# Optimization experiments

Hardware: AMD Instinct MI355X
Metric: run time of the kernel (lower is better)

Reference implementation:

```python
import jax, jax.numpy as jnp
import numpy as np

B, T, D = 256, 512, 32   # batch, seq_len, var_length (== input_size == output_size)
H, L = 256, 2            # hidden_size, num_layers


def setup_inputs() -> dict:
    key = jax.random.key(0)
    ks = jax.random.split(key, 16)
    s = 1.0 / np.sqrt(H)  # PyTorch LSTM/Linear default init range
    def u(k, shape):
        return jax.random.uniform(k, shape, jnp.float32, -s, s)
    inp = {"input": jax.random.normal(ks[0], (B, T, D), jnp.float32)}
    # encoder LSTM (b = b_ih + b_hh folded together); gate order i,f,g,o
    inp["enc_Wih0"] = u(ks[1], (4 * H, D)); inp["enc_Whh0"] = u(ks[2], (4 * H, H)); inp["enc_b0"] = u(ks[3], (4 * H,))
    inp["enc_Wih1"] = u(ks[4], (4 * H, H)); inp["enc_Whh1"] = u(ks[5], (4 * H, H)); inp["enc_b1"] = u(ks[6], (4 * H,))
    # decoder LSTM
    inp["dec_Wih0"] = u(ks[7], (4 * H, D)); inp["dec_Whh0"] = u(ks[8], (4 * H, H)); inp["dec_b0"] = u(ks[9], (4 * H,))
    inp["dec_Wih1"] = u(ks[10], (4 * H, H)); inp["dec_Whh1"] = u(ks[11], (4 * H, H)); inp["dec_b1"] = u(ks[12], (4 * H,))
    # output projection
    inp["fc_W"] = u(ks[13], (D, H)); inp["fc_b"] = u(ks[14], (D,))
    return inp


def _lstm_cell(x, h, c, Wih, Whh, b):
    g = x @ Wih.T + h @ Whh.T + b            # [B, 4H]
    i, f, gg, o = jnp.split(g, 4, axis=-1)   # PyTorch gate order i,f,g,o
    c = jax.nn.sigmoid(f) * c + jax.nn.sigmoid(i) * jnp.tanh(gg)
    h = jax.nn.sigmoid(o) * jnp.tanh(c)
    return h, c


def reference(input, enc_Wih0, enc_Whh0, enc_b0, enc_Wih1, enc_Whh1, enc_b1,
              dec_Wih0, dec_Whh0, dec_b0, dec_Wih1, dec_Whh1, dec_b1, fc_W, fc_b):
    b, t, d = input.shape
    hdim = enc_Whh0.shape[1]
    x = jnp.transpose(input, (1, 0, 2))  # time-major [T, B, D]

    # ----- encoder: 2-layer LSTM, keep final (h, c) per layer -----
    enc = [(enc_Wih0, enc_Whh0, enc_b0), (enc_Wih1, enc_Whh1, enc_b1)]
    hs, cs = [], []
    seq = x
    for Wih, Whh, bb in enc:
        def step(carry, xt, Wih=Wih, Whh=Whh, bb=bb):
            h, c = carry
            h, c = _lstm_cell(xt, h, c, Wih, Whh, bb)
            return (h, c), h
        z = jnp.zeros((b, hdim), input.dtype)
        (hT, cT), seq = jax.lax.scan(step, (z, z), seq)
        hs.append(hT); cs.append(cT)
    h0 = jnp.stack(hs)  # [L, B, H]
    c0 = jnp.stack(cs)

    dec = [(dec_Wih0, dec_Whh0, dec_b0), (dec_Wih1, dec_Whh1, dec_b1)]

    def dec_step(carry, _):
        xt, h, c = carry
        inp_l = xt
        new_h, new_c = [], []
        for l, (Wih, Whh, bb) in enumerate(dec):
            hl, cl = _lstm_cell(inp_l, h[l], c[l], Wih, Whh, bb)
            new_h.append(hl); new_c.append(cl)
            inp_l = hl
        pred = inp_l @ fc_W.T + fc_b  # [B, D]
        return (pred, jnp.stack(new_h), jnp.stack(new_c)), pred

    x0 = jnp.zeros((b, d), input.dtype)
    _, preds = jax.lax.scan(dec_step, (x0, h0, c0), None, length=t)  # [T, B, D]
    # cat along time then reverse (inv_idx)
    out = jnp.transpose(preds, (1, 0, 2))[:, ::-1, :]
    return out
```

## Files before the change

kernel.cpp:

```cpp
#include <hip/hip_runtime.h>

typedef __attribute__((ext_vector_type(8))) short bf16x8;
typedef __attribute__((ext_vector_type(4))) float f32x4;

#define MFMA16(a,b,c) __builtin_amdgcn_mfma_f32_16x16x32_bf16((a),(b),(c),0,0,0)


#define SZ_HBUF   (2*256*256*2)
#define OFF_H0H   0
#define OFF_H0L   (OFF_H0H + SZ_HBUF)
#define OFF_H1H   (OFF_H0L + SZ_HBUF)
#define OFF_H1L   (OFF_H1H + SZ_HBUF)
#define OFF_CFIN  (OFF_H1L + SZ_HBUF)
#define OFF_EW0H  (OFF_CFIN + 524288)
#define OFF_EW0L  (OFF_EW0H + 589824)
#define OFF_EW1H  (OFF_EW0L + 589824)
#define OFF_EW1L  (OFF_EW1H + 1048576)
#define OFF_DW0H  (OFF_EW1L + 1048576)
#define OFF_DW0L  (OFF_DW0H + 1048576)
#define OFF_DW1H  (OFF_DW0L + 1048576)
#define OFF_DW1L  (OFF_DW1H + 1048576)
#define OFF_BEFF  (OFF_DW1L + 1048576)
#define OFF_FCWH  (OFF_BEFF + 4096)
#define OFF_FCWL  (OFF_FCWH + 16384)
#define OFF_EFLG  (OFF_FCWL + 16384)
#define OFF_DFLG  (OFF_EFLG + 4096)

static __device__ __forceinline__ unsigned short f2bf(float f) {
  unsigned u = __float_as_uint(f);
  u = u + 0x7fffu + ((u >> 16) & 1u);
  return (unsigned short)(u >> 16);
}
static __device__ __forceinline__ float bf2f(unsigned short s) {
  return __uint_as_float(((unsigned)s) << 16);
}
static __device__ __forceinline__ float sigf(float x) {
  return 1.f / (1.f + __expf(-x));
}
static __device__ __forceinline__ float tanhsafe(float x) {
  float a = fabsf(x);
  float e = __expf(-2.f * a);
  float t = (1.f - e) / (1.f + e);
  return x < 0.f ? -t : t;
}
static __device__ __forceinline__ void st_hpair(float h, unsigned short* ph, unsigned short* pl) {
  unsigned short hi = f2bf(h);
  unsigned short lo = f2bf(h - bf2f(hi));
  __hip_atomic_store(ph, hi, __ATOMIC_RELAXED, __HIP_MEMORY_SCOPE_AGENT);
  __hip_atomic_store(pl, lo, __ATOMIC_RELAXED, __HIP_MEMORY_SCOPE_AGENT);
}
static __device__ __forceinline__ f32x4 ld16(const void* p) {
  f32x4 d;
  asm volatile("global_load_dwordx4 %0, %1, off sc0 sc1" : "=&v"(d) : "v"(p) : "memory");
  return d;
}
static __device__ __forceinline__ void wait_vm0() {
  asm volatile("s_waitcnt vmcnt(0)" ::: "memory");
  __builtin_amdgcn_sched_barrier(0);
}
static __device__ __forceinline__ void flag_barrier(unsigned* flags, int gc, unsigned round) {
  __syncthreads();
  if (threadIdx.x == 0)
    __hip_atomic_store(flags + gc, round, __ATOMIC_RELAXED, __HIP_MEMORY_SCOPE_AGENT);
  if (threadIdx.x < 64) {
    int l = threadIdx.x;
    for (;;) {
      unsigned v = (l < 16) ? __hip_atomic_load(flags + l, __ATOMIC_RELAXED, __HIP_MEMORY_SCOPE_AGENT)
                            : round;
      if (__all((int)(v >= round))) break;
    }
  }
  __syncthreads();
}

#define LDSF(base, row, kk) \
  (*(const bf16x8*)((base) + ((((row) << 9) | (lrow << 4) | ((kk) << 6)) ^ (((row) & 7) << 4))))

__global__ void k_prep_cat(int nrows, const float* __restrict__ s0, int K0,
                           const float* __restrict__ s1, int K1,
                           unsigned short* __restrict__ whi, unsigned short* __restrict__ wlo) {
  int K = K0 + K1;
  int tot = nrows * K;
  for (int idx = blockIdx.x * blockDim.x + threadIdx.x; idx < tot; idx += gridDim.x * blockDim.x) {
    int n = idx / K, k = idx - n * K;
    float v = (k < K0) ? s0[n * K0 + k] : s1[n * K1 + (k - K0)];
    unsigned short hi = f2bf(v);
    unsigned short lo = f2bf(v - bf2f(hi));
    whi[idx] = hi; wlo[idx] = lo;
  }
}
__global__ void k_prep_dec0(const float* __restrict__ Wih0, const float* __restrict__ Whh0,
                            const float* __restrict__ fcW,
                            unsigned short* __restrict__ whi, unsigned short* __restrict__ wlo) {
  int tot = 1024 * 512;
  for (int idx = blockIdx.x * blockDim.x + threadIdx.x; idx < tot; idx += gridDim.x * blockDim.x) {
    int n = idx >> 9, k = idx & 511;
    float v;
    if (k < 256) {
      v = 0.f;
      #pragma unroll
      for (int d = 0; d < 32; ++d) v += Wih0[n * 32 + d] * fcW[d * 256 + k];
    } else {
      v = Whh0[n * 256 + (k - 256)];
    }
    unsigned short hi = f2bf(v);
    unsigned short lo = f2bf(v - bf2f(hi));
    whi[idx] = hi; wlo[idx] = lo;
  }
}
__global__ void k_prep_beff(const float* __restrict__ Wih0, const float* __restrict__ b0,
                            const float* __restrict__ fcb, float* __restrict__ beff) {
  int n = blockIdx.x * blockDim.x + threadIdx.x;
  if (n < 1024) {
    float v = b0[n];
    #pragma unroll
    for (int d = 0; d < 32; ++d) v += Wih0[n * 32 + d] * fcb[d];
    beff[n] = v;
  }
}

__global__ __launch_bounds__(256, 1)
void k_encoder(const float* __restrict__ input,
               const unsigned short* __restrict__ w0hi, const unsigned short* __restrict__ w0lo,
               const unsigned short* __restrict__ w1hi, const unsigned short* __restrict__ w1lo,
               const float* __restrict__ b0, const float* __restrict__ b1,
               unsigned short* h0h, unsigned short* h0l,
               unsigned short* h1h, unsigned short* h1l,
               float* __restrict__ cfin, unsigned* flags)
{
  const int wg = blockIdx.x;
  const int gb = wg & 15, gc = wg >> 4;
  const int tid = threadIdx.x;
  const int wid = tid >> 6, lane = tid & 63;
  const int lcol = lane & 15, lrow = lane >> 4;
  const int r0 = gb * 16, u0 = gc * 16;
  const int wrow = wid * 256 + u0 + lcol;

  __shared__ char s_h0[2][8192];
  __shared__ char s_h1[2][8192];
  __shared__ float gA[4][16][17];
  __shared__ float gB[4][16][17];
  __shared__ float cb[2][16][16];

  cb[0][tid >> 4][tid & 15] = 0.f;
  cb[1][tid >> 4][tid & 15] = 0.f;

  const int srow = (tid >> 5) & 7;
  const int scol8 = (tid & 31) << 3;
  const int dA = ((srow << 9) | ((tid & 31) << 4)) ^ (srow << 4);
  const int dB = dA + 4096;

  bf16x8 w0h_[9], w0l_[9], w1h_[16], w1l_[16];
  {
    const unsigned short* p = w0hi + (size_t)wrow * 288 + lrow * 8;
    const unsigned short* q = w0lo + (size_t)wrow * 288 + lrow * 8;
    #pragma unroll
    for (int kk = 0; kk < 9; ++kk) {
      w0h_[kk] = *(const bf16x8*)(p + kk * 32);
      w0l_[kk] = *(const bf16x8*)(q + kk * 32);
    }
    const unsigned short* p1 = w1hi + (size_t)wrow * 512 + lrow * 8;
    const unsigned short* q1 = w1lo + (size_t)wrow * 512 + lrow * 8;
    #pragma unroll
    for (int kk = 0; kk < 16; ++kk) {
      w1h_[kk] = *(const bf16x8*)(p1 + kk * 32);
      w1l_[kk] = *(const bf16x8*)(q1 + kk * 32);
    }
  }
  const float bias0 = b0[wrow];
  const float bias1 = b1[wrow];
  unsigned* gflags = flags + gb * 64;
  __syncthreads();

  for (int k = 0; k <= 512; ++k) {
    const int rp = (k - 1) & 1;
    const int wp = k & 1;

    f32x4 ahh = {0.f,0.f,0.f,0.f}, ahl = {0.f,0.f,0.f,0.f}, alh = {0.f,0.f,0.f,0.f};
    union { bf16x8 v; unsigned short s[8]; } xh, xl;
    if (k < 512) {
      const float* px = input + (size_t)(r0 + lcol) * 16384 + (size_t)k * 32 + lrow * 8;
      f32x4 a = *(const f32x4*)px;
      f32x4 b = *(const f32x4*)(px + 4);
      #pragma unroll
      for (int j = 0; j < 4; ++j) {
        unsigned short t1 = f2bf(a[j]); xh.s[j] = t1;     xl.s[j]     = f2bf(a[j] - bf2f(t1));
        unsigned short t2 = f2bf(b[j]); xh.s[4 + j] = t2; xl.s[4 + j] = f2bf(b[j] - bf2f(t2));
      }
    }

    const unsigned short* p0h = h0h + (size_t)rp * 65536 + (size_t)(r0 + srow) * 256 + scol8;
    const unsigned short* p0l = h0l + (size_t)rp * 65536 + (size_t)(r0 + srow) * 256 + scol8;
    const unsigned short* p1h = h1h + (size_t)wp * 65536 + (size_t)(r0 + srow) * 256 + scol8;
    const unsigned short* p1l = h1l + (size_t)wp * 65536 + (size_t)(r0 + srow) * 256 + scol8;
    f32x4 v0 = ld16(p0h), v1 = ld16(p0h + 2048);
    f32x4 v2 = ld16(p0l), v3 = ld16(p0l + 2048);
    f32x4 v4 = ld16(p1h), v5 = ld16(p1h + 2048);
    f32x4 v6 = ld16(p1l), v7 = ld16(p1l + 2048);

    if (k < 512) {
      ahh = MFMA16(xh.v, w0h_[0], ahh);
      ahl = MFMA16(xh.v, w0l_[0], ahl);
      alh = MFMA16(xl.v, w0h_[0], alh);
    }

    wait_vm0();
    *(f32x4*)(s_h0[0] + dA) = v0; *(f32x4*)(s_h0[0] + dB) = v1;
    *(f32x4*)(s_h0[1] + dA) = v2; *(f32x4*)(s_h0[1] + dB) = v3;
    *(f32x4*)(s_h1[0] + dA) = v4; *(f32x4*)(s_h1[0] + dB) = v5;
    *(f32x4*)(s_h1[1] + dA) = v6; *(f32x4*)(s_h1[1] + dB) = v7;
    __syncthreads();

    bf16x8 f0h[8], f0l[8];
    #pragma unroll
    for (int kk = 0; kk < 8; ++kk) {
      f0h[kk] = LDSF(s_h0[0], lcol, kk);
      f0l[kk] = LDSF(s_h0[1], lcol, kk);
    }

    if (k < 512) {
      #pragma unroll
      for (int kk = 0; kk < 8; ++kk) {
        ahh = MFMA16(f0h[kk], w0h_[kk + 1], ahh);
        ahl = MFMA16(f0h[kk], w0l_[kk + 1], ahl);
        alh = MFMA16(f0l[kk], w0h_[kk + 1], alh);
      }
      f32x4 g = ahh + ahl + alh;
      #pragma unroll
      for (int r = 0; r < 4; ++r) gA[wid][lrow * 4 + r][lcol] = g[r] + bias0;
    }
    if (k >= 1) {
      f32x4 bhh = {0.f,0.f,0.f,0.f}, bhl = {0.f,0.f,0.f,0.f}, blh = {0.f,0.f,0.f,0.f};
      #pragma unroll
      for (int kk = 0; kk < 8; ++kk) {
        bhh = MFMA16(f0h[kk], w1h_[kk], bhh);
        bhl = MFMA16(f0h[kk], w1l_[kk], bhl);
        blh = MFMA16(f0l[kk], w1h_[kk], blh);
      }
      #pragma unroll
      for (int kk = 0; kk < 8; ++kk) {
        bf16x8 fh_ = LDSF(s_h1[0], lcol, kk);
        bf16x8 fl_ = LDSF(s_h1[1], lcol, kk);
        bhh = MFMA16(fh_, w1h_[kk + 8], bhh);
        bhl = MFMA16(fh_, w1l_[kk + 8], bhl);
        blh = MFMA16(fl_, w1h_[kk + 8], blh);
      }
      f32x4 g = bhh + bhl + blh;
      #pragma unroll
      for (int r = 0; r < 4; ++r) gB[wid][lrow * 4 + r][lcol] = g[r] + bias1;
    }
    __syncthreads();

    const int urow = tid >> 4, uu = tid & 15;
    if (k < 512) {
      float gi = gA[0][urow][uu], gf = gA[1][urow][uu];
      float gg = gA[2][urow][uu], go = gA[3][urow][uu];
      float c = sigf(gf) * cb[0][urow][uu] + sigf(gi) * tanhsafe(gg);
      cb[0][urow][uu] = c;
      float h = sigf(go) * tanhsafe(c);
      size_t off = (size_t)wp * 65536 + (size_t)(r0 + urow) * 256 + (u0 + uu);
      st_hpair(h, h0h + off, h0l + off);
    }
    if (k >= 1) {
      float gi = gB[0][urow][uu], gf = gB[1][urow][uu];
      float gg = gB[2][urow][uu], go = gB[3][urow][uu];
      float c = sigf(gf) * cb[1][urow][uu] + sigf(gi) * tanhsafe(gg);
      cb[1][urow][uu] = c;
      float h = sigf(go) * tanhsafe(c);
      size_t off = (size_t)rp * 65536 + (size_t)(r0 + urow) * 256 + (u0 + uu);
      st_hpair(h, h1h + off, h1l + off);
    }
    flag_barrier(gflags, gc, (unsigned)(k + 1));
  }

  const int urow = tid >> 4, uu = tid & 15;
  cfin[(size_t)(r0 + urow) * 256 + (u0 + uu)] = cb[0][urow][uu];
  cfin[65536 + (size_t)(r0 + urow) * 256 + (u0 + uu)] = cb[1][urow][uu];
}

__global__ __launch_bounds__(256, 1)
void k_decoder(const unsigned short* __restrict__ w0hi, const unsigned short* __restrict__ w0lo,
               const unsigned short* __restrict__ w1hi, const unsigned short* __restrict__ w1lo,
               const float* __restrict__ beff, const float* __restrict__ db0,
               const float* __restrict__ b1, const float* __restrict__ fcb,
               const unsigned short* __restrict__ fcwh_g, const unsigned short* __restrict__ fcwl_g,
               unsigned short* h0h, unsigned short* h0l,
               unsigned short* h1h, unsigned short* h1l,
               const float* __restrict__ cfin, float* __restrict__ out, unsigned* flags)
{
  const int wg = blockIdx.x;
  const int gb = wg & 15, gc = wg >> 4;
  const int tid = threadIdx.x;
  const int wid = tid >> 6, lane = tid & 63;
  const int lcol = lane & 15, lrow = lane >> 4;
  const int r0 = gb * 16, u0 = gc * 16;
  const int wrow = wid * 256 + u0 + lcol;

  __shared__ char s_h1[2][8192];
  __shared__ char s_h0[2][2][8192];
  __shared__ char s_fcw[2][16384];
  __shared__ float gA[4][16][17];
  __shared__ float cb[2][16][16];

  const int srow = (tid >> 5) & 7;
  const int scol8 = (tid & 31) << 3;
  const int dA = ((srow << 9) | ((tid & 31) << 4)) ^ (srow << 4);
  const int dB = dA + 4096;

  {
    const int urow = tid >> 4, uu = tid & 15;
    cb[0][urow][uu] = cfin[(size_t)(r0 + urow) * 256 + (u0 + uu)];
    cb[1][urow][uu] = cfin[65536 + (size_t)(r0 + urow) * 256 + (u0 + uu)];
  }
  {
    const unsigned short* q1h = h1h + 65536 + (size_t)(r0 + srow) * 256 + scol8;
    const unsigned short* q1l = h1l + 65536 + (size_t)(r0 + srow) * 256 + scol8;
    const unsigned short* q0h = h0h + 65536 + (size_t)(r0 + srow) * 256 + scol8;
    const unsigned short* q0l = h0l + 65536 + (size_t)(r0 + srow) * 256 + scol8;
    f32x4 v0 = ld16(q1h), v1 = ld16(q1h + 2048);
    f32x4 v2 = ld16(q1l), v3 = ld16(q1l + 2048);
    f32x4 v4 = ld16(q0h), v5 = ld16(q0h + 2048);
    f32x4 v6 = ld16(q0l), v7 = ld16(q0l + 2048);
    f32x4 fh0 = ld16(fcwh_g + (size_t)srow * 256 + scol8);
    f32x4 fh1 = ld16(fcwh_g + (size_t)(srow + 8) * 256 + scol8);
    f32x4 fh2 = ld16(fcwh_g + (size_t)(srow + 16) * 256 + scol8);
    f32x4 fh3 = ld16(fcwh_g + (size_t)(srow + 24) * 256 + scol8);
    f32x4 fl0 = ld16(fcwl_g + (size_t)srow * 256 + scol8);
    f32x4 fl1 = ld16(fcwl_g + (size_t)(srow + 8) * 256 + scol8);
    f32x4 fl2 = ld16(fcwl_g + (size_t)(srow + 16) * 256 + scol8);
    f32x4 fl3 = ld16(fcwl_g + (size_t)(srow + 24) * 256 + scol8);
    wait_vm0();
    *(f32x4*)(s_h1[0] + dA) = v0;    *(f32x4*)(s_h1[0] + dB) = v1;
    *(f32x4*)(s_h1[1] + dA) = v2;    *(f32x4*)(s_h1[1] + dB) = v3;
    *(f32x4*)(s_h0[1][0] + dA) = v4; *(f32x4*)(s_h0[1][0] + dB) = v5;
    *(f32x4*)(s_h0[1][1] + dA) = v6; *(f32x4*)(s_h0[1][1] + dB) = v7;
    *(f32x4*)(s_fcw[0] + dA) = fh0;          *(f32x4*)(s_fcw[0] + dA + 4096) = fh1;
    *(f32x4*)(s_fcw[0] + dA + 8192) = fh2;   *(f32x4*)(s_fcw[0] + dA + 12288) = fh3;
    *(f32x4*)(s_fcw[1] + dA) = fl0;          *(f32x4*)(s_fcw[1] + dA + 4096) = fl1;
    *(f32x4*)(s_fcw[1] + dA + 8192) = fl2;   *(f32x4*)(s_fcw[1] + dA + 12288) = fl3;
  }

  bf16x8 w0h_[16], w0l_[16], w1h_[16], w1l_[16];
  {
    const unsigned short* p = w0hi + (size_t)wrow * 512 + lrow * 8;
    const unsigned short* q = w0lo + (size_t)wrow * 512 + lrow * 8;
    #pragma unroll
    for (int kk = 0; kk < 16; ++kk) {
      w0h_[kk] = *(const bf16x8*)(p + kk * 32);
      w0l_[kk] = *(const bf16x8*)(q + kk * 32);
    }
    const unsigned short* p1 = w1hi + (size_t)wrow * 512 + lrow * 8;
    const unsigned short* q1 = w1lo + (size_t)wrow * 512 + lrow * 8;
    #pragma unroll
    for (int kk = 0; kk < 16; ++kk) {
      w1h_[kk] = *(const bf16x8*)(p1 + kk * 32);
      w1l_[kk] = *(const bf16x8*)(q1 + kk * 32);
    }
  }
  const float bias0 = beff[wrow], bias0t0 = db0[wrow], bias1 = b1[wrow];
  const float fcbv = (wid < 2) ? fcb[wid * 16 + lcol] : 0.f;
  unsigned* gflags = flags + gb * 64;
  __syncthreads();

  bf16x8 h1h_r[8], h1l_r[8];

  for (int t = 0; t < 512; ++t) {
    const int wp = t & 1, rp = 1 - wp;

    f32x4 a0, a1, a2, a3;
    if (t > 0) {
      const unsigned short* ph = h1h + (size_t)rp * 65536 + (size_t)(r0 + srow) * 256 + scol8;
      const unsigned short* pl = h1l + (size_t)rp * 65536 + (size_t)(r0 + srow) * 256 + scol8;
      a0 = ld16(ph); a1 = ld16(ph + 2048);
      a2 = ld16(pl); a3 = ld16(pl + 2048);
    }
    f32x4 ahh = {0.f,0.f,0.f,0.f}, ahl = {0.f,0.f,0.f,0.f}, alh = {0.f,0.f,0.f,0.f};
    #pragma unroll
    for (int kk = 0; kk < 8; ++kk) {
      bf16x8 fh_ = LDSF(s_h0[rp][0], lcol, kk);
      bf16x8 fl_ = LDSF(s_h0[rp][1], lcol, kk);
      ahh = MFMA16(fh_, w0h_[kk + 8], ahh);
      ahl = MFMA16(fh_, w0l_[kk + 8], ahl);
      alh = MFMA16(fl_, w0h_[kk + 8], alh);
    }
    if (t > 0) {
      wait_vm0();
      *(f32x4*)(s_h1[0] + dA) = a0; *(f32x4*)(s_h1[0] + dB) = a1;
      *(f32x4*)(s_h1[1] + dA) = a2; *(f32x4*)(s_h1[1] + dB) = a3;
    }
    __syncthreads();
    #pragma unroll
    for (int kk = 0; kk < 8; ++kk) {
      h1h_r[kk] = LDSF(s_h1[0], lcol, kk);
      h1l_r[kk] = LDSF(s_h1[1], lcol, kk);
    }
    if (t > 0) {
      #pragma unroll
      for (int kk = 0; kk < 8; ++kk) {
        ahh = MFMA16(h1h_r[kk], w0h_[kk], ahh);
        ahl = MFMA16(h1h_r[kk], w0l_[kk], ahl);
        alh = MFMA16(h1l_r[kk], w0h_[kk], alh);
      }
    }
    {
      f32x4 g = ahh + ahl + alh;
      float bb = (t == 0) ? bias0t0 : bias0;
      #pragma unroll
      for (int r = 0; r < 4; ++r) gA[wid][lrow * 4 + r][lcol] = g[r] + bb;
    }
    __syncthreads();
    {
      const int urow = tid >> 4, uu = tid & 15;
      float gi = gA[0][urow][uu], gf = gA[1][urow][uu];
      float gg = gA[2][urow][uu], go = gA[3][urow][uu];
      float c = sigf(gf) * cb[0][urow][uu] + sigf(gi) * tanhsafe(gg);
      cb[0][urow][uu] = c;
      float h = sigf(go) * tanhsafe(c);
      size_t off = (size_t)wp * 65536 + (size_t)(r0 + urow) * 256 + (u0 + uu);
      st_hpair(h, h0h + off, h0l + off);
    }
    flag_barrier(gflags, gc, (unsigned)(2 * t + 1));

    f32x4 b0v, b1v, b2v, b3v;
    {
      const unsigned short* ph = h0h + (size_t)wp * 65536 + (size_t)(r0 + srow) * 256 + scol8;
      const unsigned short* pl = h0l + (size_t)wp * 65536 + (size_t)(r0 + srow) * 256 + scol8;
      b0v = ld16(ph); b1v = ld16(ph + 2048);
      b2v = ld16(pl); b3v = ld16(pl + 2048);
    }
    f32x4 bhh = {0.f,0.f,0.f,0.f}, bhl = {0.f,0.f,0.f,0.f}, blh = {0.f,0.f,0.f,0.f};
    #pragma unroll
    for (int kk = 0; kk < 8; ++kk) {
      bhh = MFMA16(h1h_r[kk], w1h_[kk + 8], bhh);
      bhl = MFMA16(h1h_r[kk], w1l_[kk + 8], bhl);
      blh = MFMA16(h1l_r[kk], w1h_[kk + 8], blh);
    }
    f32x4 p0 = {0.f,0.f,0.f,0.f}, p1 = {0.f,0.f,0.f,0.f}, p2 = {0.f,0.f,0.f,0.f};
    if (t > 0 && wid < 2) {
      #pragma unroll
      for (int kk = 0; kk < 8; ++kk) {
        bf16x8 fh_ = LDSF(s_fcw[0], wid * 16 + lcol, kk);
        bf16x8 fl_ = LDSF(s_fcw[1], wid * 16 + lcol, kk);
        p0 = MFMA16(h1h_r[kk], fh_, p0);
        p1 = MFMA16(h1h_r[kk], fl_, p1);
        p2 = MFMA16(h1l_r[kk], fh_, p2);
      }
    }
    wait_vm0();
    if (t > 0 && wid < 2 && gc == 0) {
      #pragma unroll
      for (int j = 0; j < 4; ++j)
        out[(size_t)(r0 + lrow * 4 + j) * 16384 + (size_t)(512 - t) * 32 + wid * 16 + lcol] =
            p0[j] + p1[j] + p2[j] + fcbv;
    }
    *(f32x4*)(s_h0[wp][0] + dA) = b0v; *(f32x4*)(s_h0[wp][0] + dB) = b1v;
    *(f32x4*)(s_h0[wp][1] + dA) = b2v; *(f32x4*)(s_h0[wp][1] + dB) = b3v;
    __syncthreads();
    {
      #pragma unroll
      for (int kk = 0; kk < 8; ++kk) {
        bf16x8 fh_ = LDSF(s_h0[wp][0], lcol, kk);
        bf16x8 fl_ = LDSF(s_h0[wp][1], lcol, kk);
        bhh = MFMA16(fh_, w1h_[kk], bhh);
        bhl = MFMA16(fh_, w1l_[kk], bhl);
        blh = MFMA16(fl_, w1h_[kk], blh);
      }
      f32x4 g = bhh + bhl + blh;
      #pragma unroll
      for (int r = 0; r < 4; ++r) gA[wid][lrow * 4 + r][lcol] = g[r] + bias1;
    }
    __syncthreads();
    {
      const int urow = tid >> 4, uu = tid & 15;
      float gi = gA[0][urow][uu], gf = gA[1][urow][uu];
      float gg = gA[2][urow][uu], go = gA[3][urow][uu];
      float c = sigf(gf) * cb[1][urow][uu] + sigf(gi) * tanhsafe(gg);
      cb[1][urow][uu] = c;
      float h = sigf(go) * tanhsafe(c);
      size_t off = (size_t)wp * 65536 + (size_t)(r0 + urow) * 256 + (u0 + uu);
      st_hpair(h, h1h + off, h1l + off);
    }
    flag_barrier(gflags, gc, (unsigned)(2 * t + 2));
  }

  {
    const unsigned short* ph = h1h + 65536 + (size_t)(r0 + srow) * 256 + scol8;
    const unsigned short* pl = h1l + 65536 + (size_t)(r0 + srow) * 256 + scol8;
    f32x4 v0 = ld16(ph), v1 = ld16(ph + 2048);
    f32x4 v2 = ld16(pl), v3 = ld16(pl + 2048);
    wait_vm0();
    *(f32x4*)(s_h1[0] + dA) = v0; *(f32x4*)(s_h1[0] + dB) = v1;
    *(f32x4*)(s_h1[1] + dA) = v2; *(f32x4*)(s_h1[1] + dB) = v3;
  }
  __syncthreads();
  if (wid < 2) {
    f32x4 p0 = {0.f,0.f,0.f,0.f}, p1 = {0.f,0.f,0.f,0.f}, p2 = {0.f,0.f,0.f,0.f};
    #pragma unroll
    for (int kk = 0; kk < 8; ++kk) {
      bf16x8 ah = LDSF(s_h1[0], lcol, kk);
      bf16x8 al = LDSF(s_h1[1], lcol, kk);
      bf16x8 fh_ = LDSF(s_fcw[0], wid * 16 + lcol, kk);
      bf16x8 fl_ = LDSF(s_fcw[1], wid * 16 + lcol, kk);
      p0 = MFMA16(ah, fh_, p0);
      p1 = MFMA16(ah, fl_, p1);
      p2 = MFMA16(al, fh_, p2);
    }
    if (gc == 0) {
      #pragma unroll
      for (int j = 0; j < 4; ++j)
        out[(size_t)(r0 + lrow * 4 + j) * 16384 + wid * 16 + lcol] = p0[j] + p1[j] + p2[j] + fcbv;
    }
  }
}

extern "C" void kernel_launch(void* const* d_in, const int* in_sizes, int n_in,
                              void* d_out, int out_size, void* d_ws, size_t ws_size,
                              hipStream_t stream) {
  (void)in_sizes; (void)n_in; (void)ws_size;
  const float* input = (const float*)d_in[0];
  const float* eWih0 = (const float*)d_in[1];
  const float* eWhh0 = (const float*)d_in[2];
  const float* eb0   = (const float*)d_in[3];
  const float* eWih1 = (const float*)d_in[4];
  const float* eWhh1 = (const float*)d_in[5];
  const float* eb1   = (const float*)d_in[6];
  const float* dWih0 = (const float*)d_in[7];
  const float* dWhh0 = (const float*)d_in[8];
  const float* db0   = (const float*)d_in[9];
  const float* dWih1 = (const float*)d_in[10];
  const float* dWhh1 = (const float*)d_in[11];
  const float* db1   = (const float*)d_in[12];
  const float* fcW   = (const float*)d_in[13];
  const float* fcb   = (const float*)d_in[14];

  char* ws = (char*)d_ws;
  unsigned short* h0h = (unsigned short*)(ws + OFF_H0H);
  unsigned short* h0l = (unsigned short*)(ws + OFF_H0L);
  unsigned short* h1h = (unsigned short*)(ws + OFF_H1H);
  unsigned short* h1l = (unsigned short*)(ws + OFF_H1L);
  float* cfin = (float*)(ws + OFF_CFIN);
  unsigned short* ew0h = (unsigned short*)(ws + OFF_EW0H);
  unsigned short* ew0l = (unsigned short*)(ws + OFF_EW0L);
  unsigned short* ew1h = (unsigned short*)(ws + OFF_EW1H);
  unsigned short* ew1l = (unsigned short*)(ws + OFF_EW1L);
  unsigned short* dw0h = (unsigned short*)(ws + OFF_DW0H);
  unsigned short* dw0l = (unsigned short*)(ws + OFF_DW0L);
  unsigned short* dw1h = (unsigned short*)(ws + OFF_DW1H);
  unsigned short* dw1l = (unsigned short*)(ws + OFF_DW1L);
  float* beff = (float*)(ws + OFF_BEFF);
  unsigned short* fcwh = (unsigned short*)(ws + OFF_FCWH);
  unsigned short* fcwl = (unsigned short*)(ws + OFF_FCWL);
  unsigned* eflg = (unsigned*)(ws + OFF_EFLG);
  unsigned* dflg = (unsigned*)(ws + OFF_DFLG);

  hipMemsetAsync(d_out, 0, (size_t)out_size * sizeof(float), stream);
  hipMemsetAsync(ws + OFF_H0H, 0, (size_t)4 * SZ_HBUF, stream);
  hipMemsetAsync(ws + OFF_EFLG, 0, 8192, stream);

  k_prep_cat<<<1024, 256, 0, stream>>>(1024, eWih0, 32,  eWhh0, 256, ew0h, ew0l);
  k_prep_cat<<<1024, 256, 0, stream>>>(1024, eWih1, 256, eWhh1, 256, ew1h, ew1l);
  k_prep_cat<<<1024, 256, 0, stream>>>(1024, dWih1, 256, dWhh1, 256, dw1h, dw1l);
  k_prep_cat<<<64, 256, 0, stream>>>(32, fcW, 256, fcW, 0, fcwh, fcwl);
  k_prep_dec0<<<1024, 256, 0, stream>>>(dWih0, dWhh0, fcW, dw0h, dw0l);
  k_prep_beff<<<4, 256, 0, stream>>>(dWih0, db0, fcb, beff);

  k_encoder<<<256, 256, 0, stream>>>(input, ew0h, ew0l, ew1h, ew1l, eb0, eb1,
                                     h0h, h0l, h1h, h1l, cfin, eflg);
  k_decoder<<<256, 256, 0, stream>>>(dw0h, dw0l, dw1h, dw1l, beff, db0, db1, fcb,
                                     fcwh, fcwl, h0h, h0l, h1h, h1l, cfin,
                                     (float*)d_out, dflg);
}
```

Measured before the change: 4.125 ms.

## Replace block-level flag barrier with per-wave publish/wait flags and register cell state

```diff
diff --git a/kernel.cpp b/kernel.cpp
--- a/kernel.cpp
+++ b/kernel.cpp
@@ -54,23 +54,27 @@
   asm volatile("global_load_dwordx4 %0, %1, off sc0 sc1" : "=&v"(d) : "v"(p) : "memory");
   return d;
 }
+static __device__ __forceinline__ f32x4 ld16nc(const void* p) {
+  f32x4 d;
+  asm volatile("global_load_dwordx4 %0, %1, off" : "=&v"(d) : "v"(p) : "memory");
+  return d;
+}
 static __device__ __forceinline__ void wait_vm0() {
   asm volatile("s_waitcnt vmcnt(0)" ::: "memory");
   __builtin_amdgcn_sched_barrier(0);
 }
-static __device__ __forceinline__ void flag_barrier(unsigned* flags, int gc, unsigned round) {
-  __syncthreads();
-  if (threadIdx.x == 0)
-    __hip_atomic_store(flags + gc, round, __ATOMIC_RELAXED, __HIP_MEMORY_SCOPE_AGENT);
-  if (threadIdx.x < 64) {
-    int l = threadIdx.x;
-    for (;;) {
-      unsigned v = (l < 16) ? __hip_atomic_load(flags + l, __ATOMIC_RELAXED, __HIP_MEMORY_SCOPE_AGENT)
-                            : round;
-      if (__all((int)(v >= round))) break;
-    }
-  }
-  __syncthreads();
+static __device__ __forceinline__ void wave_publish(unsigned* wf, int slot, unsigned round) {
+  asm volatile("s_waitcnt vmcnt(0)" ::: "memory");
+  __builtin_amdgcn_sched_barrier(0);
+  if ((threadIdx.x & 63) == 0)
+    __hip_atomic_store(wf + slot, round, __ATOMIC_RELAXED, __HIP_MEMORY_SCOPE_AGENT);
+}
+static __device__ __forceinline__ void wave_wait(const unsigned* wf, unsigned round) {
+  int l = threadIdx.x & 63;
+  for (;;) {
+    unsigned v = __hip_atomic_load(wf + l, __ATOMIC_RELAXED, __HIP_MEMORY_SCOPE_AGENT);
+    if (__all((int)(v >= round))) break;
+  }
 }
 
 #define LDSF(base, row, kk) \
@@ -135,15 +139,12 @@
   const int lcol = lane & 15, lrow = lane >> 4;
   const int r0 = gb * 16, u0 = gc * 16;
   const int wrow = wid * 256 + u0 + lcol;
+  const int urow = tid >> 4, uu = tid & 15;
 
   __shared__ char s_h0[2][8192];
   __shared__ char s_h1[2][8192];
   __shared__ float gA[4][16][17];
   __shared__ float gB[4][16][17];
-  __shared__ float cb[2][16][16];
-
-  cb[0][tid >> 4][tid & 15] = 0.f;
-  cb[1][tid >> 4][tid & 15] = 0.f;
 
   const int srow = (tid >> 5) & 7;
   const int scol8 = (tid & 31) << 3;
@@ -169,25 +170,26 @@
   }
   const float bias0 = b0[wrow];
   const float bias1 = b1[wrow];
+  float c0reg = 0.f, c1reg = 0.f;
   unsigned* gflags = flags + gb * 64;
+  const int wslot = gc * 4 + wid;
+
+  const float* pxrow = input + (size_t)(r0 + lcol) * 16384 + lrow * 8;
+  union { bf16x8 v; unsigned short s[8]; } xh, xl;
+  {
+    f32x4 a = *(const f32x4*)(pxrow);
+    f32x4 b = *(const f32x4*)(pxrow + 4);
+    #pragma unroll
+    for (int j = 0; j < 4; ++j) {
+      unsigned short t1 = f2bf(a[j]); xh.s[j] = t1;     xl.s[j]     = f2bf(a[j] - bf2f(t1));
+      unsigned short t2 = f2bf(b[j]); xh.s[4 + j] = t2; xl.s[4 + j] = f2bf(b[j] - bf2f(t2));
+    }
+  }
   __syncthreads();
 
   for (int k = 0; k <= 512; ++k) {
     const int rp = (k - 1) & 1;
     const int wp = k & 1;
-
-    f32x4 ahh = {0.f,0.f,0.f,0.f}, ahl = {0.f,0.f,0.f,0.f}, alh = {0.f,0.f,0.f,0.f};
-    union { bf16x8 v; unsigned short s[8]; } xh, xl;
-    if (k < 512) {
-      const float* px = input + (size_t)(r0 + lcol) * 16384 + (size_t)k * 32 + lrow * 8;
-      f32x4 a = *(const f32x4*)px;
-      f32x4 b = *(const f32x4*)(px + 4);
-      #pragma unroll
-      for (int j = 0; j < 4; ++j) {
-        unsigned short t1 = f2bf(a[j]); xh.s[j] = t1;     xl.s[j]     = f2bf(a[j] - bf2f(t1));
-        unsigned short t2 = f2bf(b[j]); xh.s[4 + j] = t2; xl.s[4 + j] = f2bf(b[j] - bf2f(t2));
-      }
-    }
 
     const unsigned short* p0h = h0h + (size_t)rp * 65536 + (size_t)(r0 + srow) * 256 + scol8;
     const unsigned short* p0l = h0l + (size_t)rp * 65536 + (size_t)(r0 + srow) * 256 + scol8;
@@ -197,7 +199,13 @@
     f32x4 v2 = ld16(p0l), v3 = ld16(p0l + 2048);
     f32x4 v4 = ld16(p1h), v5 = ld16(p1h + 2048);
     f32x4 v6 = ld16(p1l), v7 = ld16(p1l + 2048);
-
+    f32x4 nxa, nxb;
+    if (k < 511) {
+      nxa = ld16nc(pxrow + (size_t)(k + 1) * 32);
+      nxb = ld16nc(pxrow + (size_t)(k + 1) * 32 + 4);
+    }
+
+    f32x4 ahh = {0.f,0.f,0.f,0.f}, ahl = {0.f,0.f,0.f,0.f}, alh = {0.f,0.f,0.f,0.f};
     if (k < 512) {
       ahh = MFMA16(xh.v, w0h_[0], ahh);
       ahl = MFMA16(xh.v, w0l_[0], ahl);
@@ -209,6 +217,13 @@
     *(f32x4*)(s_h0[1] + dA) = v2; *(f32x4*)(s_h0[1] + dB) = v3;
     *(f32x4*)(s_h1[0] + dA) = v4; *(f32x4*)(s_h1[0] + dB) = v5;
     *(f32x4*)(s_h1[1] + dA) = v6; *(f32x4*)(s_h1[1] + dB) = v7;
+    if (k < 511) {
+      #pragma unroll
+      for (int j = 0; j < 4; ++j) {
+        unsigned short t1 = f2bf(nxa[j]); xh.s[j] = t1;     xl.s[j]     = f2bf(nxa[j] - bf2f(t1));
+        unsigned short t2 = f2bf(nxb[j]); xh.s[4 + j] = t2; xl.s[4 + j] = f2bf(nxb[j] - bf2f(t2));
+      }
+    }
     __syncthreads();
 
     bf16x8 f0h[8], f0l[8];
@@ -251,12 +266,11 @@
     }
     __syncthreads();
 
-    const int urow = tid >> 4, uu = tid & 15;
     if (k < 512) {
       float gi = gA[0][urow][uu], gf = gA[1][urow][uu];
       float gg = gA[2][urow][uu], go = gA[3][urow][uu];
-      float c = sigf(gf) * cb[0][urow][uu] + sigf(gi) * tanhsafe(gg);
-      cb[0][urow][uu] = c;
+      float c = sigf(gf) * c0reg + sigf(gi) * tanhsafe(gg);
+      c0reg = c;
       float h = sigf(go) * tanhsafe(c);
       size_t off = (size_t)wp * 65536 + (size_t)(r0 + urow) * 256 + (u0 + uu);
       st_hpair(h, h0h + off, h0l + off);
@@ -264,18 +278,18 @@
     if (k >= 1) {
       float gi = gB[0][urow][uu], gf = gB[1][urow][uu];
       float gg = gB[2][urow][uu], go = gB[3][urow][uu];
-      float c = sigf(gf) * cb[1][urow][uu] + sigf(gi) * tanhsafe(gg);
-      cb[1][urow][uu] = c;
+      float c = sigf(gf) * c1reg + sigf(gi) * tanhsafe(gg);
+      c1reg = c;
       float h = sigf(go) * tanhsafe(c);
       size_t off = (size_t)rp * 65536 + (size_t)(r0 + urow) * 256 + (u0 + uu);
       st_hpair(h, h1h + off, h1l + off);
     }
-    flag_barrier(gflags, gc, (unsigned)(k + 1));
-  }
-
-  const int urow = tid >> 4, uu = tid & 15;
-  cfin[(size_t)(r0 + urow) * 256 + (u0 + uu)] = cb[0][urow][uu];
-  cfin[65536 + (size_t)(r0 + urow) * 256 + (u0 + uu)] = cb[1][urow][uu];
+    wave_publish(gflags, wslot, (unsigned)(k + 1));
+    wave_wait(gflags, (unsigned)(k + 1));
+  }
+
+  cfin[(size_t)(r0 + urow) * 256 + (u0 + uu)] = c0reg;
+  cfin[65536 + (size_t)(r0 + urow) * 256 + (u0 + uu)] = c1reg;
 }
 
 __global__ __launch_bounds__(256, 1)
@@ -295,40 +309,39 @@
   const int lcol = lane & 15, lrow = lane >> 4;
   const int r0 = gb * 16, u0 = gc * 16;
   const int wrow = wid * 256 + u0 + lcol;
+  const int urow = tid >> 4, uu = tid & 15;
 
   __shared__ char s_h1[2][8192];
   __shared__ char s_h0[2][2][8192];
   __shared__ char s_fcw[2][16384];
   __shared__ float gA[4][16][17];
-  __shared__ float cb[2][16][16];
 
   const int srow = (tid >> 5) & 7;
   const int scol8 = (tid & 31) << 3;
   const int dA = ((srow << 9) | ((tid & 31) << 4)) ^ (srow << 4);
   const int dB = dA + 4096;
 
+  float c0reg = cfin[(size_t)(r0 + urow) * 256 + (u0 + uu)];
+  float c1reg = cfin[65536 + (size_t)(r0 + urow) * 256 + (u0 + uu)];
+
+  const size_t rowoff = (size_t)(r0 + srow) * 256 + scol8;
   {
-    const int urow = tid >> 4, uu = tid & 15;
-    cb[0][urow][uu] = cfin[(size_t)(r0 + urow) * 256 + (u0 + uu)];
-    cb[1][urow][uu] = cfin[65536 + (size_t)(r0 + urow) * 256 + (u0 + uu)];
-  }
-  {
-    const unsigned short* q1h = h1h + 65536 + (size_t)(r0 + srow) * 256 + scol8;
-    const unsigned short* q1l = h1l + 65536 + (size_t)(r0 + srow) * 256 + scol8;
-    const unsigned short* q0h = h0h + 65536 + (size_t)(r0 + srow) * 256 + scol8;
-    const unsigned short* q0l = h0l + 65536 + (size_t)(r0 + srow) * 256 + scol8;
+    const unsigned short* q1h = h1h + 65536 + rowoff;
+    const unsigned short* q1l = h1l + 65536 + rowoff;
+    const unsigned short* q0h = h0h + 65536 + rowoff;
+    const unsigned short* q0l = h0l + 65536 + rowoff;
     f32x4 v0 = ld16(q1h), v1 = ld16(q1h + 2048);
     f32x4 v2 = ld16(q1l), v3 = ld16(q1l + 2048);
     f32x4 v4 = ld16(q0h), v5 = ld16(q0h + 2048);
     f32x4 v6 = ld16(q0l), v7 = ld16(q0l + 2048);
-    f32x4 fh0 = ld16(fcwh_g + (size_t)srow * 256 + scol8);
-    f32x4 fh1 = ld16(fcwh_g + (size_t)(srow + 8) * 256 + scol8);
-    f32x4 fh2 = ld16(fcwh_g + (size_t)(srow + 16) * 256 + scol8);
-    f32x4 fh3 = ld16(fcwh_g + (size_t)(srow + 24) * 256 + scol8);
-    f32x4 fl0 = ld16(fcwl_g + (size_t)srow * 256 + scol8);
-    f32x4 fl1 = ld16(fcwl_g + (size_t)(srow + 8) * 256 + scol8);
-    f32x4 fl2 = ld16(fcwl_g + (size_t)(srow + 16) * 256 + scol8);
-    f32x4 fl3 = ld16(fcwl_g + (size_t)(srow + 24) * 256 + scol8);
+    f32x4 fh0 = ld16nc(fcwh_g + (size_t)srow * 256 + scol8);
+    f32x4 fh1 = ld16nc(fcwh_g + (size_t)(srow + 8) * 256 + scol8);
+    f32x4 fh2 = ld16nc(fcwh_g + (size_t)(srow + 16) * 256 + scol8);
+    f32x4 fh3 = ld16nc(fcwh_g + (size_t)(srow + 24) * 256 + scol8);
+    f32x4 fl0 = ld16nc(fcwl_g + (size_t)srow * 256 + scol8);
+    f32x4 fl1 = ld16nc(fcwl_g + (size_t)(srow + 8) * 256 + scol8);
+    f32x4 fl2 = ld16nc(fcwl_g + (size_t)(srow + 16) * 256 + scol8);
+    f32x4 fl3 = ld16nc(fcwl_g + (size_t)(srow + 24) * 256 + scol8);
     wait_vm0();
     *(f32x4*)(s_h1[0] + dA) = v0;    *(f32x4*)(s_h1[0] + dB) = v1;
     *(f32x4*)(s_h1[1] + dA) = v2;    *(f32x4*)(s_h1[1] + dB) = v3;
@@ -360,6 +373,11 @@
   const float bias0 = beff[wrow], bias0t0 = db0[wrow], bias1 = b1[wrow];
   const float fcbv = (wid < 2) ? fcb[wid * 16 + lcol] : 0.f;
   unsigned* gflags = flags + gb * 64;
+  const int wslot = gc * 4 + wid;
+  const unsigned short* h1h_p0 = h1h + rowoff; const unsigned short* h1h_p1 = h1h + 65536 + rowoff;
+  const unsigned short* h1l_p0 = h1l + rowoff; const unsigned short* h1l_p1 = h1l + 65536 + rowoff;
+  const unsigned short* h0h_p0 = h0h + rowoff; const unsigned short* h0h_p1 = h0h + 65536 + rowoff;
+  const unsigned short* h0l_p0 = h0l + rowoff; const unsigned short* h0l_p1 = h0l + 65536 + rowoff;
   __syncthreads();
 
   bf16x8 h1h_r[8], h1l_r[8];
@@ -369,8 +387,8 @@
 
     f32x4 a0, a1, a2, a3;
     if (t > 0) {
-      const unsigned short* ph = h1h + (size_t)rp * 65536 + (size_t)(r0 + srow) * 256 + scol8;
-      const unsigned short* pl = h1l + (size_t)rp * 65536 + (size_t)(r0 + srow) * 256 + scol8;
+      const unsigned short* ph = rp ? h1h_p1 : h1h_p0;
+      const unsigned short* pl = rp ? h1l_p1 : h1l_p0;
       a0 = ld16(ph); a1 = ld16(ph + 2048);
       a2 = ld16(pl); a3 = ld16(pl + 2048);
     }
@@ -410,21 +428,21 @@
     }
     __syncthreads();
     {
-      const int urow = tid >> 4, uu = tid & 15;
       float gi = gA[0][urow][uu], gf = gA[1][urow][uu];
       float gg = gA[2][urow][uu], go = gA[3][urow][uu];
-      float c = sigf(gf) * cb[0][urow][uu] + sigf(gi) * tanhsafe(gg);
-      cb[0][urow][uu] = c;
+      float c = sigf(gf) * c0reg + sigf(gi) * tanhsafe(gg);
+      c0reg = c;
       float h = sigf(go) * tanhsafe(c);
       size_t off = (size_t)wp * 65536 + (size_t)(r0 + urow) * 256 + (u0 + uu);
       st_hpair(h, h0h + off, h0l + off);
     }
-    flag_barrier(gflags, gc, (unsigned)(2 * t + 1));
+    wave_publish(gflags, wslot, (unsigned)(2 * t + 1));
+    wave_wait(gflags, (unsigned)(2 * t + 1));
 
     f32x4 b0v, b1v, b2v, b3v;
     {
-      const unsigned short* ph = h0h + (size_t)wp * 65536 + (size_t)(r0 + srow) * 256 + scol8;
-      const unsigned short* pl = h0l + (size_t)wp * 65536 + (size_t)(r0 + srow) * 256 + scol8;
+      const unsigned short* ph = wp ? h0h_p1 : h0h_p0;
+      const unsigned short* pl = wp ? h0l_p1 : h0l_p0;
       b0v = ld16(ph); b1v = ld16(ph + 2048);
       b2v = ld16(pl); b3v = ld16(pl + 2048);
     }
@@ -471,23 +489,21 @@
     }
     __syncthreads();
     {
-      const int urow = tid >> 4, uu = tid & 15;
       float gi = gA[0][urow][uu], gf = gA[1][urow][uu];
       float gg = gA[2][urow][uu], go = gA[3][urow][uu];
-      float c = sigf(gf) * cb[1][urow][uu] + sigf(gi) * tanhsafe(gg);
-      cb[1][urow][uu] = c;
+      float c = sigf(gf) * c1reg + sigf(gi) * tanhsafe(gg);
+      c1reg = c;
       float h = sigf(go) * tanhsafe(c);
       size_t off = (size_t)wp * 65536 + (size_t)(r0 + urow) * 256 + (u0 + uu);
       st_hpair(h, h1h + off, h1l + off);
     }
-    flag_barrier(gflags, gc, (unsigned)(2 * t + 2));
+    wave_publish(gflags, wslot, (unsigned)(2 * t + 2));
+    wave_wait(gflags, (unsigned)(2 * t + 2));
   }
 
   {
-    const unsigned short* ph = h1h + 65536 + (size_t)(r0 + srow) * 256 + scol8;
-    const unsigned short* pl = h1l + 65536 + (size_t)(r0 + srow) * 256 + scol8;
-    f32x4 v0 = ld16(ph), v1 = ld16(ph + 2048);
-    f32x4 v2 = ld16(pl), v3 = ld16(pl + 2048);
+    f32x4 v0 = ld16(h1h_p1), v1 = ld16(h1h_p1 + 2048);
+    f32x4 v2 = ld16(h1l_p1), v3 = ld16(h1l_p1 + 2048);
     wait_vm0();
     *(f32x4*)(s_h1[0] + dA) = v0; *(f32x4*)(s_h1[0] + dB) = v1;
     *(f32x4*)(s_h1[1] + dA) = v2; *(f32x4*)(s_h1[1] + dB) = v3;
```

Result: slower. 12.69 ms (+207.7%).
